# Performance work log

Measured on AMD Instinct MI355X. Metric: run time of the kernel, lower is better.

## Reference

```python
import jax, jax.numpy as jnp
import numpy as np

N_EXPERTS = 8
TOPK = 2
D_MODEL = 2048
D_FF = 2048
N_TOKENS = 8192
FP8_MAX = 448.0  # float8_e4m3fn max


def _fp8_quant_scalar(w):
    # per-tensor (scalar) fp8 quantization, as fp8_quantize(weight, scalar=True)
    amax = jnp.max(jnp.abs(w))
    scale = jnp.maximum(amax, 1e-12) / FP8_MAX
    q = (w / scale).astype(jnp.float8_e4m3fn).astype(jnp.float32)
    return q, scale


def _fp8_qdq_st(x):
    # dynamic_quant(x, single_scale=True) followed by inline dequant,
    # with straight-through estimator so fwd/bwd modules share math.
    amax = jnp.max(jnp.abs(x))
    scale = jnp.maximum(amax, 1e-12) / FP8_MAX
    qdq = (x / scale).astype(jnp.float8_e4m3fn).astype(jnp.float32) * scale
    return x + jax.lax.stop_gradient(qdq - x)


def setup_inputs() -> dict:
    key = jax.random.key(0)
    k1, k2, k3, k4 = jax.random.split(key, 4)
    x = jax.random.normal(k1, (N_TOKENS, D_MODEL), dtype=jnp.float32)
    gating_output = jax.random.normal(k2, (N_TOKENS, N_EXPERTS), dtype=jnp.float32)
    # per-expert fused gate+up weight [E, 2*d_ff, d_model], down weight [E, d_model, d_ff]
    w13 = jax.random.normal(k3, (N_EXPERTS, 2 * D_FF, D_MODEL), dtype=jnp.float32) * 0.02
    w2 = jax.random.normal(k4, (N_EXPERTS, D_MODEL, D_FF), dtype=jnp.float32) * 0.02
    w13_q, w13_scale = jax.vmap(_fp8_quant_scalar)(w13)
    w2_q, w2_scale = jax.vmap(_fp8_quant_scalar)(w2)
    return {
        "x": x,
        "gating_output": gating_output,
        "w13_q": w13_q,
        "w13_scale": w13_scale,
        "w2_q": w2_q,
        "w2_scale": w2_scale,
    }


def reference(x, gating_output, w13_q, w13_scale, w2_q, w2_scale):
    # --- select_experts: softmax scoring, top-k, renormalize ---
    probs = jax.nn.softmax(gating_output, axis=-1)              # [T, E]
    topk_w, topk_ids = jax.lax.top_k(probs, TOPK)               # [T, K]
    topk_w = topk_w / jnp.sum(topk_w, axis=-1, keepdims=True)   # renormalize=True

    # --- dynamic fp8 quantize + dequant of hidden states (single scale) ---
    x_dq = _fp8_qdq_st(x)                                       # [T, D]

    out = jnp.zeros((x.shape[0], D_MODEL), dtype=jnp.float32)
    for e in range(N_EXPERTS):
        # combine weight per token for this expert
        combine = jnp.sum(jnp.where(topk_ids == e, topk_w, 0.0), axis=-1)  # [T]
        w13 = w13_q[e] * w13_scale[e]                            # dequant [2F, D]
        w2 = w2_q[e] * w2_scale[e]                               # dequant [D, F]
        gu = x_dq @ w13.T                                        # [T, 2F]
        gate, up = gu[:, :D_FF], gu[:, D_FF:]
        h = jax.nn.silu(gate) * up                               # [T, F]
        out = out + combine[:, None] * (h @ w2.T)                # [T, D]
    return out
```

## Files before the change

kernel.cpp:

```cpp
#include <hip/hip_runtime.h>
#include <stdint.h>

#define T_TOK 8192
#define DM    2048
#define DFF   2048

typedef __attribute__((ext_vector_type(8))) short bf16x8;
typedef __attribute__((ext_vector_type(4))) float f32x4;
typedef __attribute__((ext_vector_type(4))) int   i32x4;
typedef __attribute__((ext_vector_type(8))) int   i32x8;

#define OFF_AMAX  0
#define OFF_CNT   64
#define OFF_PBASE 128
#define OFF_TMETA 192
#define OFF_TSE   256
#define OFF_TM0   960
#define OFF_BTOK  4096
#define OFF_BW    (OFF_BTOK + 16*T_TOK*4)
#define OFF_XQ    (2*1024*1024)
#define OFF_W13F  (OFF_XQ + T_TOK*DM)
#define OFF_W2B   (OFF_W13F + 8*2*DFF*DM)
#define OFF_H     (OFF_W2B + 8*DM*DFF*2)

#define GP(p) ((const __attribute__((address_space(1))) void*)(uintptr_t)(p))
#define LP(p) ((__attribute__((address_space(3))) void*)(uint32_t)(uintptr_t)(p))

__device__ __forceinline__ short bf16_rne(float f) {
    uint32_t b = __float_as_uint(f);
    b += 0x7FFFu + ((b >> 16) & 1u);
    return (short)(b >> 16);
}

__device__ __forceinline__ float fp8_round(float y) {
    float a = fabsf(y);
    a = fminf(a, 448.f);
    uint32_t b = __float_as_uint(a);
    if (b >= 0x3C800000u) {
        uint32_t lsb = (b >> 20) & 1u;
        b += 0x7FFFFu + lsb;
        b &= 0xFFF00000u;
        a = __uint_as_float(b);
    } else {
        a = rintf(a * 512.f) * (1.f / 512.f);
    }
    return (y < 0.f) ? -a : a;
}

__device__ __forceinline__ unsigned char fp8_enc(float v) {
    uint32_t b = __float_as_uint(v);
    uint32_t s = (b >> 24) & 0x80u;
    float a = fabsf(v);
    uint32_t q;
    if (a < 0.015625f) {
        q = (uint32_t)(a * 512.0f + 0.5f);
    } else {
        uint32_t e = (b >> 23) & 0xFFu;
        uint32_t m = (b >> 20) & 7u;
        q = ((e - 120u) << 3) | m;
    }
    return (unsigned char)(s | q);
}

__global__ void k_amax(const float4* __restrict__ x, unsigned* __restrict__ amax) {
    __shared__ float red[256];
    float m = 0.f;
    const int n4 = T_TOK * DM / 4;
    for (int i = blockIdx.x * blockDim.x + threadIdx.x; i < n4; i += gridDim.x * blockDim.x) {
        float4 v = x[i];
        m = fmaxf(m, fmaxf(fmaxf(fabsf(v.x), fabsf(v.y)), fmaxf(fabsf(v.z), fabsf(v.w))));
    }
    red[threadIdx.x] = m;
    __syncthreads();
    for (int s = 128; s > 0; s >>= 1) {
        if (threadIdx.x < s) red[threadIdx.x] = fmaxf(red[threadIdx.x], red[threadIdx.x + s]);
        __syncthreads();
    }
    if (threadIdx.x == 0) atomicMax(amax, __float_as_uint(red[0]));
}

__global__ void k_router(const float* __restrict__ gating, int* __restrict__ cnt,
                         int* __restrict__ btok, float* __restrict__ bw) {
    __shared__ int lcnt[16];
    __shared__ int lbase[16];
    const int tid = threadIdx.x;
    if (tid < 16) lcnt[tid] = 0;
    __syncthreads();
    const int t = blockIdx.x * 256 + tid;
    float l[8], p[8];
    float lmax = -1e30f;
#pragma unroll
    for (int i = 0; i < 8; i++) { l[i] = gating[t * 8 + i]; lmax = fmaxf(lmax, l[i]); }
    float s = 0.f;
#pragma unroll
    for (int i = 0; i < 8; i++) { p[i] = __expf(l[i] - lmax); s += p[i]; }
    int i0 = 0;
#pragma unroll
    for (int i = 1; i < 8; i++) if (l[i] > l[i0]) i0 = i;
    int i1 = (i0 == 0) ? 1 : 0;
#pragma unroll
    for (int i = 0; i < 8; i++) if (i != i1 && i != i0 && l[i] > l[i1]) i1 = i;
    float pa = p[i0] / s, pb = p[i1] / s;
    float w0 = pa / (pa + pb), w1 = pb / (pa + pb);
    int p0 = atomicAdd(&lcnt[i0], 1);
    int p1 = atomicAdd(&lcnt[8 + i1], 1);
    __syncthreads();
    if (tid < 16) lbase[tid] = atomicAdd(&cnt[tid], lcnt[tid]);
    __syncthreads();
    int pos = lbase[i0] + p0;
    btok[i0 * T_TOK + pos] = t; bw[i0 * T_TOK + pos] = w0;
    pos = lbase[8 + i1] + p1;
    btok[(8 + i1) * T_TOK + pos] = t; bw[(8 + i1) * T_TOK + pos] = w1;
}

__global__ void k_build(const int* __restrict__ cnt, int* __restrict__ pbase,
                        int* __restrict__ tmeta, int* __restrict__ tse, int* __restrict__ tm0) {
    if (threadIdx.x != 0 || blockIdx.x != 0) return;
    int base = 0, tt = 0, t0 = 0;
    for (int b = 0; b < 16; b++) {
        pbase[b] = base;
        int nt = (cnt[b] + 127) >> 7;
        for (int i = 0; i < nt; i++) { tse[tt] = b; tm0[tt] = i << 7; tt++; }
        base += nt << 7;
        if (b == 7) t0 = tt;
    }
    tmeta[0] = t0; tmeta[1] = tt;
}

__global__ void k_quant(const float4* __restrict__ x, unsigned char* __restrict__ xq,
                        const unsigned* __restrict__ amax) {
    float scale = fmaxf(__uint_as_float(*amax), 1e-12f) / 448.f;
    const int n4 = T_TOK * DM / 4;
    for (int i = blockIdx.x * blockDim.x + threadIdx.x; i < n4; i += gridDim.x * blockDim.x) {
        float4 v = x[i];
        uchar4 o;
        o.x = fp8_enc(fp8_round(v.x / scale));
        o.y = fp8_enc(fp8_round(v.y / scale));
        o.z = fp8_enc(fp8_round(v.z / scale));
        o.w = fp8_enc(fp8_round(v.w / scale));
        ((uchar4*)xq)[i] = o;
    }
}

__global__ void k_conv13(const float4* __restrict__ w, unsigned char* __restrict__ o, int n4) {
    for (int i = blockIdx.x * blockDim.x + threadIdx.x; i < n4; i += gridDim.x * blockDim.x) {
        float4 v = w[i];
        uchar4 q;
        q.x = fp8_enc(v.x); q.y = fp8_enc(v.y); q.z = fp8_enc(v.z); q.w = fp8_enc(v.w);
        ((uchar4*)o)[i] = q;
    }
}

__global__ void k_conv(const float4* __restrict__ w, short* __restrict__ o, int n4) {
    for (int i = blockIdx.x * blockDim.x + threadIdx.x; i < n4; i += gridDim.x * blockDim.x) {
        float4 v = w[i];
        short4 q;
        q.x = bf16_rne(v.x); q.y = bf16_rne(v.y); q.z = bf16_rne(v.z); q.w = bf16_rne(v.w);
        ((short4*)o)[i] = q;
    }
}

__launch_bounds__(256, 2)
__global__ void k_gemm1(const unsigned char* __restrict__ xq, const unsigned char* __restrict__ w13f,
                        short* __restrict__ hbuf, const char* __restrict__ ws,
                        const float* __restrict__ w13_scale) {
    const int* cnt   = (const int*)(ws + OFF_CNT);
    const int* pbase = (const int*)(ws + OFF_PBASE);
    const int* tmeta = (const int*)(ws + OFF_TMETA);
    const int* tse   = (const int*)(ws + OFF_TSE);
    const int* tm0a  = (const int*)(ws + OFF_TM0);
    const int* btok  = (const int*)(ws + OFF_BTOK);
    const float* bwt = (const float*)(ws + OFF_BW);

    int ti = blockIdx.y;
    if (ti >= tmeta[1]) return;
    const int b = tse[ti], m0 = tm0a[ti], e = b & 7, c_n = cnt[b];
    const int hbase = pbase[b] + m0;
    const int n0 = blockIdx.x * 64;

    const int tid = threadIdx.x, w = tid >> 6, l = tid & 63;
    __shared__ i32x4 smv[2048];
    char* sm = (char*)smv;

    const int rb = w * 8 + (l >> 3);
    const int gchunk = (l & 7) ^ (l >> 3);
    const int* btk = btok + b * T_TOK;
    const unsigned char* ap[4];
    const unsigned char* bp[4];
#pragma unroll
    for (int c = 0; c < 4; c++) {
        int r = c * 32 + rb;
        int rr = m0 + r; if (rr >= c_n) rr = c_n - 1;
        ap[c] = xq + (size_t)btk[rr] * DM + gchunk * 16;
        int wr = (r < 64) ? (n0 + r) : (DFF + n0 + (r - 64));
        bp[c] = w13f + (size_t)e * (2 * DFF) * DM + (size_t)wr * DM + gchunk * 16;
    }

    f32x4 zero = {0.f, 0.f, 0.f, 0.f};
    f32x4 acc[4][4];
#pragma unroll
    for (int i = 0; i < 4; i++)
#pragma unroll
        for (int j = 0; j < 4; j++) acc[i][j] = zero;

    const int mw = w & 1, nw = w >> 1;
    const int fr = l & 15, fk = l >> 4;

    for (int kt = 0; kt < 16; kt++) {
        const int ko = kt * 128;
#pragma unroll
        for (int c = 0; c < 4; c++)
            __builtin_amdgcn_global_load_lds(GP(ap[c] + ko), LP(sm + c * 4096 + w * 1024), 16, 0, 0);
#pragma unroll
        for (int c = 0; c < 4; c++)
            __builtin_amdgcn_global_load_lds(GP(bp[c] + ko), LP(sm + 16384 + c * 4096 + w * 1024), 16, 0, 0);
        asm volatile("s_waitcnt vmcnt(0)" ::: "memory");
        __syncthreads();

        i32x8 af[4], bf[4];
#pragma unroll
        for (int i = 0; i < 4; i++) {
            int row = mw * 64 + i * 16 + fr;
            const char* base = sm + row * 128;
            i32x4 lo = *(const i32x4*)(base + ((((fk * 2)) ^ (row & 7)) << 4));
            i32x4 hi = *(const i32x4*)(base + ((((fk * 2) | 1) ^ (row & 7)) << 4));
            af[i][0] = lo[0]; af[i][1] = lo[1]; af[i][2] = lo[2]; af[i][3] = lo[3];
            af[i][4] = hi[0]; af[i][5] = hi[1]; af[i][6] = hi[2]; af[i][7] = hi[3];
        }
#pragma unroll
        for (int j = 0; j < 4; j++) {
            int row = nw * 64 + j * 16 + fr;
            const char* base = sm + 16384 + row * 128;
            i32x4 lo = *(const i32x4*)(base + ((((fk * 2)) ^ (row & 7)) << 4));
            i32x4 hi = *(const i32x4*)(base + ((((fk * 2) | 1) ^ (row & 7)) << 4));
            bf[j][0] = lo[0]; bf[j][1] = lo[1]; bf[j][2] = lo[2]; bf[j][3] = lo[3];
            bf[j][4] = hi[0]; bf[j][5] = hi[1]; bf[j][6] = hi[2]; bf[j][7] = hi[3];
        }
#pragma unroll
        for (int i = 0; i < 4; i++)
#pragma unroll
            for (int j = 0; j < 4; j++)
                acc[i][j] = __builtin_amdgcn_mfma_scale_f32_16x16x128_f8f6f4(
                    af[i], bf[j], acc[i][j], 0, 0, 0, 0x7F7F7F7F, 0, 0x7F7F7F7F);
        __syncthreads();
    }

    const float sx = fmaxf(__uint_as_float(*(const unsigned*)(ws + OFF_AMAX)), 1e-12f) / 448.f;
    const float s1 = sx * w13_scale[e];
    float* U = (float*)sm;
    if (nw == 1) {
#pragma unroll
        for (int i = 0; i < 4; i++)
#pragma unroll
            for (int j = 0; j < 4; j++)
#pragma unroll
                for (int r = 0; r < 4; r++) {
                    int lm = i * 16 + fk * 4 + r, col = j * 16 + fr;
                    U[mw * 4096 + lm * 64 + col] = acc[i][j][r];
                }
    }
    __syncthreads();
    if (nw == 0) {
#pragma unroll
        for (int i = 0; i < 4; i++)
#pragma unroll
            for (int j = 0; j < 4; j++)
#pragma unroll
                for (int r = 0; r < 4; r++) {
                    int lml = i * 16 + fk * 4 + r;
                    int lm = mw * 64 + lml, col = j * 16 + fr;
                    float g = acc[i][j][r] * s1;
                    float u = U[mw * 4096 + lml * 64 + col] * s1;
                    float cc = (m0 + lm < c_n) ? bwt[b * T_TOK + m0 + lm] : 0.f;
                    float h = g / (1.f + __expf(-g)) * u * cc;
                    hbuf[(size_t)(hbase + lm) * DFF + n0 + col] = bf16_rne(h);
                }
    }
}

__launch_bounds__(256, 2)
__global__ void k_gemm2(const short* __restrict__ hbuf, const short* __restrict__ w2b,
                        float* __restrict__ out, const char* __restrict__ ws,
                        const float* __restrict__ w2_scale, const int slot) {
    const int* cnt   = (const int*)(ws + OFF_CNT);
    const int* pbase = (const int*)(ws + OFF_PBASE);
    const int* tmeta = (const int*)(ws + OFF_TMETA);
    const int* tse   = (const int*)(ws + OFF_TSE);
    const int* tm0a  = (const int*)(ws + OFF_TM0);
    const int* btok  = (const int*)(ws + OFF_BTOK);

    const int lo = slot ? tmeta[0] : 0;
    const int hi = slot ? tmeta[1] : tmeta[0];
    int ti = lo + blockIdx.y;
    if (ti >= hi) return;
    const int b = tse[ti], m0 = tm0a[ti], e = b & 7, c_n = cnt[b];
    const int hb = pbase[b] + m0;
    const int n0 = blockIdx.x * 128;

    const int tid = threadIdx.x, w = tid >> 6, l = tid & 63;
    __shared__ i32x4 smv2[2048];
    short* sm = (short*)smv2;

    const int rb = w * 8 + (l >> 3);
    const int gchunk = (l & 7) ^ (l >> 3);
    const short* ap[4];
    const short* bp[4];
#pragma unroll
    for (int c = 0; c < 4; c++) {
        int r = c * 32 + rb;
        ap[c] = hbuf + (size_t)(hb + r) * DFF + gchunk * 8;
        bp[c] = w2b + (size_t)e * DM * DFF + (size_t)(n0 + r) * DFF + gchunk * 8;
    }

    f32x4 zero = {0.f, 0.f, 0.f, 0.f};
    f32x4 acc[4][4];
#pragma unroll
    for (int i = 0; i < 4; i++)
#pragma unroll
        for (int j = 0; j < 4; j++) acc[i][j] = zero;

    const int mw = w & 1, nw = w >> 1;
    const int fr = l & 15, fk = l >> 4;

    for (int kt = 0; kt < 32; kt++) {
        const int ko = kt * 64;
#pragma unroll
        for (int c = 0; c < 4; c++)
            __builtin_amdgcn_global_load_lds(GP(ap[c] + ko), LP(sm + c * 2048 + w * 512), 16, 0, 0);
#pragma unroll
        for (int c = 0; c < 4; c++)
            __builtin_amdgcn_global_load_lds(GP(bp[c] + ko), LP(sm + 8192 + c * 2048 + w * 512), 16, 0, 0);
        asm volatile("s_waitcnt vmcnt(0)" ::: "memory");
        __syncthreads();
#pragma unroll
        for (int kk = 0; kk < 2; kk++) {
            const int g = kk * 4 + fk;
            bf16x8 af[4], bfr[4];
#pragma unroll
            for (int i = 0; i < 4; i++) {
                int row = mw * 64 + i * 16 + fr;
                af[i] = *(const bf16x8*)&sm[row * 64 + ((g ^ (row & 7)) << 3)];
            }
#pragma unroll
            for (int j = 0; j < 4; j++) {
                int row = nw * 64 + j * 16 + fr;
                bfr[j] = *(const bf16x8*)&sm[8192 + row * 64 + ((g ^ (row & 7)) << 3)];
            }
#pragma unroll
            for (int i = 0; i < 4; i++)
#pragma unroll
                for (int j = 0; j < 4; j++)
                    acc[i][j] = __builtin_amdgcn_mfma_f32_16x16x32_bf16(af[i], bfr[j], acc[i][j], 0, 0, 0);
        }
        __syncthreads();
    }

    const float s2 = w2_scale[e];
#pragma unroll
    for (int i = 0; i < 4; i++)
#pragma unroll
        for (int r = 0; r < 4; r++) {
            int lm = mw * 64 + i * 16 + fk * 4 + r;
            if (m0 + lm < c_n) {
                int tok = btok[b * T_TOK + m0 + lm];
#pragma unroll
                for (int j = 0; j < 4; j++) {
                    int col = n0 + nw * 64 + j * 16 + fr;
                    float v = acc[i][j][r] * s2;
                    float* o = out + (size_t)tok * DM + col;
                    if (slot) *o += v; else *o = v;
                }
            }
        }
}

extern "C" void kernel_launch(void* const* d_in, const int* in_sizes, int n_in,
                              void* d_out, int out_size, void* d_ws, size_t ws_size,
                              hipStream_t stream) {
    const float* x      = (const float*)d_in[0];
    const float* gating = (const float*)d_in[1];
    const float* w13q   = (const float*)d_in[2];
    const float* w13s   = (const float*)d_in[3];
    const float* w2q    = (const float*)d_in[4];
    const float* w2s    = (const float*)d_in[5];
    float* out = (float*)d_out;
    char* ws = (char*)d_ws;

    hipMemsetAsync(ws, 0, 4096, stream);
    k_amax<<<1024, 256, 0, stream>>>((const float4*)x, (unsigned*)(ws + OFF_AMAX));
    k_router<<<T_TOK / 256, 256, 0, stream>>>(gating, (int*)(ws + OFF_CNT),
                                              (int*)(ws + OFF_BTOK), (float*)(ws + OFF_BW));
    k_build<<<1, 64, 0, stream>>>((const int*)(ws + OFF_CNT), (int*)(ws + OFF_PBASE),
                                  (int*)(ws + OFF_TMETA), (int*)(ws + OFF_TSE), (int*)(ws + OFF_TM0));
    k_quant<<<1024, 256, 0, stream>>>((const float4*)x, (unsigned char*)(ws + OFF_XQ),
                                      (const unsigned*)(ws + OFF_AMAX));
    k_conv13<<<2048, 256, 0, stream>>>((const float4*)w13q, (unsigned char*)(ws + OFF_W13F),
                                       8 * 2 * DFF * DM / 4);
    k_conv<<<1024, 256, 0, stream>>>((const float4*)w2q, (short*)(ws + OFF_W2B), 8 * DM * DFF / 4);
    k_gemm1<<<dim3(32, 144), 256, 0, stream>>>((const unsigned char*)(ws + OFF_XQ),
                                               (const unsigned char*)(ws + OFF_W13F),
                                               (short*)(ws + OFF_H), ws, w13s);
    k_gemm2<<<dim3(16, 72), 256, 0, stream>>>((const short*)(ws + OFF_H), (const short*)(ws + OFF_W2B),
                                              out, ws, w2s, 0);
    k_gemm2<<<dim3(16, 72), 256, 0, stream>>>((const short*)(ws + OFF_H), (const short*)(ws + OFF_W2B),
                                              out, ws, w2s, 1);
}
```

Baseline: 987.7 us.

## Merge gemm2 slot launches with atomic output, parallelize build, permute fp8 LDS chunks

The two sequential gemm2 launches, one per top-k slot, become a single launch over all tiles. Output is zeroed with a memset and accumulated with float atomicAdd, which removes a serial dependency and doubles the grid for better occupancy, at the cost of an extra memset and atomic traffic. k_build now parallelizes tile metadata generation across threads. gemm1 also permutes the global-to-LDS chunk mapping so each lane's fp8 fragment is read as chunks pc and pc^4, changing the LDS access pattern.

```diff
diff --git a/kernel.cpp b/kernel.cpp
--- a/kernel.cpp
+++ b/kernel.cpp
@@ -115,16 +115,28 @@
 
 __global__ void k_build(const int* __restrict__ cnt, int* __restrict__ pbase,
                         int* __restrict__ tmeta, int* __restrict__ tse, int* __restrict__ tm0) {
-    if (threadIdx.x != 0 || blockIdx.x != 0) return;
-    int base = 0, tt = 0, t0 = 0;
-    for (int b = 0; b < 16; b++) {
-        pbase[b] = base;
-        int nt = (cnt[b] + 127) >> 7;
-        for (int i = 0; i < nt; i++) { tse[tt] = b; tm0[tt] = i << 7; tt++; }
-        base += nt << 7;
-        if (b == 7) t0 = tt;
-    }
-    tmeta[0] = t0; tmeta[1] = tt;
+    __shared__ int nt[16], rbase[16], tstart[17];
+    const int tid = threadIdx.x;
+    if (tid < 16) nt[tid] = (cnt[tid] + 127) >> 7;
+    __syncthreads();
+    if (tid == 0) {
+        int b = 0, t = 0;
+        for (int i = 0; i < 16; i++) {
+            rbase[i] = b; tstart[i] = t;
+            b += nt[i] << 7; t += nt[i];
+        }
+        tstart[16] = t;
+        tmeta[0] = tstart[8]; tmeta[1] = t;
+    }
+    __syncthreads();
+    if (tid < 16) pbase[tid] = rbase[tid];
+    const int tt = tstart[16];
+    if (tid < tt) {
+        int b = 0;
+        while (tstart[b + 1] <= tid) b++;
+        tse[tid] = b;
+        tm0[tid] = (tid - tstart[b]) << 7;
+    }
 }
 
 __global__ void k_quant(const float4* __restrict__ x, unsigned char* __restrict__ xq,
@@ -183,7 +195,8 @@
     char* sm = (char*)smv;
 
     const int rb = w * 8 + (l >> 3);
-    const int gchunk = (l & 7) ^ (l >> 3);
+    const int s8 = (l & 7) ^ (l >> 3);
+    const int gchunk = (s8 < 4) ? (s8 << 1) : ((s8 << 1) - 7);
     const int* btk = btok + b * T_TOK;
     const unsigned char* ap[4];
     const unsigned char* bp[4];
@@ -222,8 +235,9 @@
         for (int i = 0; i < 4; i++) {
             int row = mw * 64 + i * 16 + fr;
             const char* base = sm + row * 128;
-            i32x4 lo = *(const i32x4*)(base + ((((fk * 2)) ^ (row & 7)) << 4));
-            i32x4 hi = *(const i32x4*)(base + ((((fk * 2) | 1) ^ (row & 7)) << 4));
+            int pc = fk ^ (row & 7);
+            i32x4 lo = *(const i32x4*)(base + (pc << 4));
+            i32x4 hi = *(const i32x4*)(base + ((pc ^ 4) << 4));
             af[i][0] = lo[0]; af[i][1] = lo[1]; af[i][2] = lo[2]; af[i][3] = lo[3];
             af[i][4] = hi[0]; af[i][5] = hi[1]; af[i][6] = hi[2]; af[i][7] = hi[3];
         }
@@ -231,8 +245,9 @@
         for (int j = 0; j < 4; j++) {
             int row = nw * 64 + j * 16 + fr;
             const char* base = sm + 16384 + row * 128;
-            i32x4 lo = *(const i32x4*)(base + ((((fk * 2)) ^ (row & 7)) << 4));
-            i32x4 hi = *(const i32x4*)(base + ((((fk * 2) | 1) ^ (row & 7)) << 4));
+            int pc = fk ^ (row & 7);
+            i32x4 lo = *(const i32x4*)(base + (pc << 4));
+            i32x4 hi = *(const i32x4*)(base + ((pc ^ 4) << 4));
             bf[j][0] = lo[0]; bf[j][1] = lo[1]; bf[j][2] = lo[2]; bf[j][3] = lo[3];
             bf[j][4] = hi[0]; bf[j][5] = hi[1]; bf[j][6] = hi[2]; bf[j][7] = hi[3];
         }
@@ -281,7 +296,7 @@
 __launch_bounds__(256, 2)
 __global__ void k_gemm2(const short* __restrict__ hbuf, const short* __restrict__ w2b,
                         float* __restrict__ out, const char* __restrict__ ws,
-                        const float* __restrict__ w2_scale, const int slot) {
+                        const float* __restrict__ w2_scale) {
     const int* cnt   = (const int*)(ws + OFF_CNT);
     const int* pbase = (const int*)(ws + OFF_PBASE);
     const int* tmeta = (const int*)(ws + OFF_TMETA);
@@ -289,10 +304,8 @@
     const int* tm0a  = (const int*)(ws + OFF_TM0);
     const int* btok  = (const int*)(ws + OFF_BTOK);
 
-    const int lo = slot ? tmeta[0] : 0;
-    const int hi = slot ? tmeta[1] : tmeta[0];
-    int ti = lo + blockIdx.y;
-    if (ti >= hi) return;
+    int ti = blockIdx.y;
+    if (ti >= tmeta[1]) return;
     const int b = tse[ti], m0 = tm0a[ti], e = b & 7, c_n = cnt[b];
     const int hb = pbase[b] + m0;
     const int n0 = blockIdx.x * 128;
@@ -366,9 +379,7 @@
 #pragma unroll
                 for (int j = 0; j < 4; j++) {
                     int col = n0 + nw * 64 + j * 16 + fr;
-                    float v = acc[i][j][r] * s2;
-                    float* o = out + (size_t)tok * DM + col;
-                    if (slot) *o += v; else *o = v;
+                    atomicAdd(out + (size_t)tok * DM + col, acc[i][j][r] * s2);
                 }
             }
         }
@@ -387,11 +398,12 @@
     char* ws = (char*)d_ws;
 
     hipMemsetAsync(ws, 0, 4096, stream);
+    hipMemsetAsync(out, 0, (size_t)T_TOK * DM * sizeof(float), stream);
     k_amax<<<1024, 256, 0, stream>>>((const float4*)x, (unsigned*)(ws + OFF_AMAX));
     k_router<<<T_TOK / 256, 256, 0, stream>>>(gating, (int*)(ws + OFF_CNT),
                                               (int*)(ws + OFF_BTOK), (float*)(ws + OFF_BW));
-    k_build<<<1, 64, 0, stream>>>((const int*)(ws + OFF_CNT), (int*)(ws + OFF_PBASE),
-                                  (int*)(ws + OFF_TMETA), (int*)(ws + OFF_TSE), (int*)(ws + OFF_TM0));
+    k_build<<<1, 256, 0, stream>>>((const int*)(ws + OFF_CNT), (int*)(ws + OFF_PBASE),
+                                   (int*)(ws + OFF_TMETA), (int*)(ws + OFF_TSE), (int*)(ws + OFF_TM0));
     k_quant<<<1024, 256, 0, stream>>>((const float4*)x, (unsigned char*)(ws + OFF_XQ),
                                       (const unsigned*)(ws + OFF_AMAX));
     k_conv13<<<2048, 256, 0, stream>>>((const float4*)w13q, (unsigned char*)(ws + OFF_W13F),
@@ -400,8 +412,6 @@
     k_gemm1<<<dim3(32, 144), 256, 0, stream>>>((const unsigned char*)(ws + OFF_XQ),
                                                (const unsigned char*)(ws + OFF_W13F),
                                                (short*)(ws + OFF_H), ws, w13s);
-    k_gemm2<<<dim3(16, 72), 256, 0, stream>>>((const short*)(ws + OFF_H), (const short*)(ws + OFF_W2B),
-                                              out, ws, w2s, 0);
-    k_gemm2<<<dim3(16, 72), 256, 0, stream>>>((const short*)(ws + OFF_H), (const short*)(ws + OFF_W2B),
-                                              out, ws, w2s, 1);
-}
+    k_gemm2<<<dim3(16, 144), 256, 0, stream>>>((const short*)(ws + OFF_H), (const short*)(ws + OFF_W2B),
+                                               out, ws, w2s);
+}
```

Result: faster. 946.9 us (-4.1%).
